# Performance work log

Measured on AMD Instinct MI355X. Metric: run time of the kernel, lower is better.

## Reference

```python
import jax, jax.numpy as jnp
import numpy as np
import math

N_GENES = 5000
N_FREQ = 10
D_EMB = 5
D_SINE = N_FREQ * 2 * 2  # 40


def _sine_consts():
    i = jnp.arange(1, N_FREQ + 1, dtype=jnp.float32)
    freqs = jnp.repeat(1.0 / 1000.0 ** (2.0 * i / N_FREQ), 2)  # [2*n_freq]
    shifts = jnp.tile(jnp.array([0.0, math.pi / 2], dtype=jnp.float32), N_FREQ)  # [2*n_freq]
    return freqs, shifts


def setup_inputs() -> dict:
    key = jax.random.key(0)
    k1, k2, k3 = jax.random.split(key, 3)
    N = 1000000
    coordinates = jax.random.normal(k1, (N, 2), dtype=jnp.float32)
    gene_ix = jax.random.randint(k2, (N,), 0, N_GENES, dtype=jnp.int64) if jax.config.jax_enable_x64 else jax.random.randint(k2, (N,), 0, N_GENES, dtype=jnp.int32)
    stdv = 1.0 / math.sqrt(D_EMB)
    weight1 = jax.random.uniform(k3, (N_GENES, D_SINE, D_EMB), dtype=jnp.float32, minval=-stdv, maxval=stdv)
    bias1 = jnp.zeros((N_GENES, D_EMB), dtype=jnp.float32)
    return {"coordinates": coordinates, "gene_ix": gene_ix, "weight1": weight1, "bias1": bias1}


def reference(coordinates, gene_ix, weight1, bias1):
    freqs, shifts = _sine_consts()
    # [N, 2, 2*n_freq] -> [N, 4*n_freq]
    emb = jnp.sin(coordinates[..., None] * freqs + shifts).reshape(coordinates.shape[0], -1)
    w = weight1[gene_ix]              # [N, D_SINE, D_EMB] gather
    b = bias1[gene_ix]                # [N, D_EMB]
    out = jnp.einsum('ab,abc->ac', emb, w) + b
    return jax.nn.sigmoid(out)
```

## Files before the change

kernel.cpp:

```cpp
#include <hip/hip_runtime.h>
#include <hip/hip_bf16.h>
#include <math.h>


#define N_GENES 5000
#define BLK_BYTES 128
#define W5_BYTES ((size_t)N_GENES * BLK_BYTES)
#define GENES_PER_BLK 51

typedef _Float16 half2_t __attribute__((ext_vector_type(2)));

#if __has_builtin(__builtin_amdgcn_fdot2)
__device__ __forceinline__ float fdot2f(half2_t a, half2_t b, float c) {
    return __builtin_amdgcn_fdot2(a, b, c, false);
}
#else
__device__ __forceinline__ float fdot2f(half2_t a, half2_t b, float c) {
    return fmaf((float)a.x, (float)b.x, fmaf((float)a.y, (float)b.y, c));
}
#endif

__device__ __forceinline__ half2_t pkrtz(float a, float b) {
    auto r = __builtin_amdgcn_cvt_pkrtz(a, b);
    union { decltype(r) s; half2_t d; } v; v.s = r; return v.d;
}
__device__ __forceinline__ half2_t u2h(unsigned int u) {
    union { unsigned int i; half2_t h; } v; v.i = u; return v.h;
}
__device__ __forceinline__ float u2f(unsigned int u) {
    union { unsigned int i; float f; } v; v.i = u; return v.f;
}
__device__ __forceinline__ unsigned int h2u(_Float16 lo, _Float16 hi) {
    union { _Float16 h[2]; unsigned int i; } v; v.h[0] = lo; v.h[1] = hi; return v.i;
}
__device__ __forceinline__ unsigned int f2u(float f) {
    union { float f; unsigned int i; } v; v.f = f; return v.i;
}

__device__ __constant__ float FRc[10] = {
    0.251188643150958f, 0.0630957344480193f, 0.0158489319246111f,
    0.00398107170553497f, 0.001f, 0.000251188643150958f,
    6.30957344480193e-05f, 1.58489319246111e-05f, 3.98107170553497e-06f, 1e-06f
};

__global__ __launch_bounds__(256) void build_w5_lds(
    const float* __restrict__ w,
    const float* __restrict__ bias,
    unsigned char* __restrict__ w5)
{
    __shared__ float lds[GENES_PER_BLK * 200];
    const int g0 = blockIdx.x * GENES_PER_BLK;
    const int ng = (N_GENES - g0 < GENES_PER_BLK) ? (N_GENES - g0) : GENES_PER_BLK;

    const float4* __restrict__ src =
        reinterpret_cast<const float4*>(w + (size_t)g0 * 200);
    const int nf4 = ng * 50;
    for (int k = threadIdx.x; k < nf4; k += 256)
        reinterpret_cast<float4*>(lds)[k] = src[k];
    __syncthreads();

    const int u = threadIdx.x;
    if (u >= ng * 5) return;
    const int gl = u / 5, c = u - 5 * gl;
    const int g = g0 + gl;
    const float* base = lds + gl * 200 + c;

    uint4 S;
    S.x = h2u((_Float16)base[0 * 5],  (_Float16)base[1 * 5]);
    S.y = h2u((_Float16)base[2 * 5],  (_Float16)base[3 * 5]);
    S.z = h2u((_Float16)base[20 * 5], (_Float16)base[21 * 5]);
    S.w = h2u((_Float16)base[22 * 5], (_Float16)base[23 * 5]);

    float Lx = 0.f, Ly = 0.f;
    float bp = bias[(size_t)g * 5 + c];
#pragma unroll
    for (int i = 2; i < 10; ++i) {
        Lx += FRc[i] * base[(2 * i) * 5];
        Ly += FRc[i] * base[(20 + 2 * i) * 5];
        bp += base[(2 * i + 1) * 5] + base[(21 + 2 * i) * 5];
    }

    unsigned char* blk = w5 + (size_t)g * BLK_BYTES;
    *reinterpret_cast<uint4*>(blk + c * 16) = S;
    uint2 L;
    L.x = h2u((_Float16)Lx, (_Float16)Ly);
    L.y = f2u(bp);
    *reinterpret_cast<uint2*>(blk + 80 + c * 8) = L;
}

template <int I>
__device__ __forceinline__ half2_t sc_pack(float x) {
    float t = x * FRc[I];
    float s, co;
    if (I == 0) {
        s  = __sinf(t);
        co = __cosf(t);
    } else {
        float u = t * t;
        s  = t * fmaf(u, fmaf(u, 1.f / 120.f, -1.f / 6.f), 1.f);
        co = fmaf(u, fmaf(u, 1.f / 24.f, -0.5f), 1.f);
    }
    return pkrtz(s, co);
}

__global__ __launch_bounds__(1024) void frag_embed5(
    const float* __restrict__ coords,
    const int*   __restrict__ gene_ix,
    const unsigned char* __restrict__ w5,
    float*       __restrict__ out,
    unsigned int N)
{
    unsigned int tid = blockIdx.x * 1024u + threadIdx.x;
    unsigned int n = tid / 5u;
    unsigned int c = tid - n * 5u;
    if (n >= N) return;

    const float x = coords[2 * (size_t)n];
    const float y = coords[2 * (size_t)n + 1];
    const int g = gene_ix[n];

    const unsigned char* __restrict__ blk = w5 + (size_t)g * BLK_BYTES;
    const uint4 S = *reinterpret_cast<const uint4*>(blk + c * 16);
    const uint2 L = *reinterpret_cast<const uint2*>(blk + 80 + c * 8);

    half2_t sx0 = sc_pack<0>(x), sx1 = sc_pack<1>(x);
    half2_t sy0 = sc_pack<0>(y), sy1 = sc_pack<1>(y);
    half2_t xy  = pkrtz(x, y);

    float acc = u2f(L.y);
    acc = fdot2f(sx0, u2h(S.x), acc);
    acc = fdot2f(sx1, u2h(S.y), acc);
    acc = fdot2f(sy0, u2h(S.z), acc);
    acc = fdot2f(sy1, u2h(S.w), acc);
    acc = fdot2f(xy,  u2h(L.x), acc);

    float r = 1.f / (1.f + __expf(-acc));
    __builtin_nontemporal_store(r, out + (size_t)n * 5 + c);
}

__global__ __launch_bounds__(256) void frag_embed_fallback(
    const float* __restrict__ coords, const int* __restrict__ gene_ix,
    const float* __restrict__ weight, const float* __restrict__ bias,
    float* __restrict__ out, int N)
{
    int n = blockIdx.x * blockDim.x + threadIdx.x;
    if (n >= N) return;
    const float cxo = coords[2 * (size_t)n];
    const float cyo = coords[2 * (size_t)n + 1];
    const int g = gene_ix[n];
    float emb[40];
    float c2[2] = { cxo, cyo };
#pragma unroll
    for (int d = 0; d < 2; ++d)
#pragma unroll
        for (int i = 0; i < 10; ++i) {
            float t = c2[d] * FRc[i];
            emb[d * 20 + 2 * i]     = __sinf(t);
            emb[d * 20 + 2 * i + 1] = __cosf(t);
        }
    const float4* wp = reinterpret_cast<const float4*>(weight + (size_t)g * 200);
    float acc[5];
#pragma unroll
    for (int c = 0; c < 5; ++c) acc[c] = bias[(size_t)g * 5 + c];
#pragma unroll
    for (int j = 0; j < 50; ++j) {
        float4 wv = wp[j];
        const int k = 4 * j;
        acc[(k + 0) % 5] = fmaf(emb[(k + 0) / 5], wv.x, acc[(k + 0) % 5]);
        acc[(k + 1) % 5] = fmaf(emb[(k + 1) / 5], wv.y, acc[(k + 1) % 5]);
        acc[(k + 2) % 5] = fmaf(emb[(k + 2) / 5], wv.z, acc[(k + 2) % 5]);
        acc[(k + 3) % 5] = fmaf(emb[(k + 3) / 5], wv.w, acc[(k + 3) % 5]);
    }
    size_t ob = (size_t)n * 5;
#pragma unroll
    for (int c = 0; c < 5; ++c)
        out[ob + c] = 1.f / (1.f + __expf(-acc[c]));
}

extern "C" void kernel_launch(void* const* d_in, const int* in_sizes, int n_in,
                              void* d_out, int out_size, void* d_ws, size_t ws_size,
                              hipStream_t stream) {
    const float* coords = (const float*)d_in[0];
    const int*   gene   = (const int*)d_in[1];
    const float* w      = (const float*)d_in[2];
    const float* b      = (const float*)d_in[3];
    float*       out    = (float*)d_out;
    const int N = in_sizes[1];

    if (ws_size >= W5_BYTES) {
        unsigned char* w5 = (unsigned char*)d_ws;
        int rblocks = (N_GENES + GENES_PER_BLK - 1) / GENES_PER_BLK;
        build_w5_lds<<<rblocks, 256, 0, stream>>>(w, b, w5);
        long long threads = (long long)N * 5;
        int grid = (int)((threads + 1023) / 1024);
        frag_embed5<<<grid, 1024, 0, stream>>>(coords, gene, w5, out, (unsigned)N);
    } else {
        frag_embed_fallback<<<(N + 255) / 256, 256, 0, stream>>>(coords, gene, w, b, out, N);
    }
}
```

Before: 21.56 us.

## Share per-row sine/cos computation across channel threads via LDS

The main kernel now launches 5x64 thread blocks. Four of the five channel threads per row each compute one sin/cos pair with the hardware intrinsics and write it to shared memory. The other threads read these values after a barrier instead of each computing the sin/cos plus a polynomial approximation itself. Weights and bias are stored negated so the sigmoid becomes rcp(1+exp(acc)) without a negation. The cost is a __syncthreads, LDS traffic, 5-wide thread rows that pack poorly into 64-lane wavefronts, and a precision change: the second frequency now uses __sinf/__cosf instead of the Taylor polynomial.

```diff
diff --git a/kernel.cpp b/kernel.cpp
--- a/kernel.cpp
+++ b/kernel.cpp
@@ -29,6 +29,9 @@
 }
 __device__ __forceinline__ float u2f(unsigned int u) {
     union { unsigned int i; float f; } v; v.i = u; return v.f;
+}
+__device__ __forceinline__ unsigned int h2uu(half2_t h) {
+    union { half2_t h; unsigned int i; } v; v.h = h; return v.i;
 }
 __device__ __forceinline__ unsigned int h2u(_Float16 lo, _Float16 hi) {
     union { _Float16 h[2]; unsigned int i; } v; v.h[0] = lo; v.h[1] = hi; return v.i;
@@ -66,10 +69,10 @@
     const float* base = lds + gl * 200 + c;
 
     uint4 S;
-    S.x = h2u((_Float16)base[0 * 5],  (_Float16)base[1 * 5]);
-    S.y = h2u((_Float16)base[2 * 5],  (_Float16)base[3 * 5]);
-    S.z = h2u((_Float16)base[20 * 5], (_Float16)base[21 * 5]);
-    S.w = h2u((_Float16)base[22 * 5], (_Float16)base[23 * 5]);
+    S.x = h2u((_Float16)(-base[0 * 5]),  (_Float16)(-base[1 * 5]));
+    S.y = h2u((_Float16)(-base[2 * 5]),  (_Float16)(-base[3 * 5]));
+    S.z = h2u((_Float16)(-base[20 * 5]), (_Float16)(-base[21 * 5]));
+    S.w = h2u((_Float16)(-base[22 * 5]), (_Float16)(-base[23 * 5]));
 
     float Lx = 0.f, Ly = 0.f;
     float bp = bias[(size_t)g * 5 + c];
@@ -83,59 +86,57 @@
     unsigned char* blk = w5 + (size_t)g * BLK_BYTES;
     *reinterpret_cast<uint4*>(blk + c * 16) = S;
     uint2 L;
-    L.x = h2u((_Float16)Lx, (_Float16)Ly);
-    L.y = f2u(bp);
+    L.x = h2u((_Float16)(-Lx), (_Float16)(-Ly));
+    L.y = f2u(-bp);
     *reinterpret_cast<uint2*>(blk + 80 + c * 8) = L;
 }
 
-template <int I>
-__device__ __forceinline__ half2_t sc_pack(float x) {
-    float t = x * FRc[I];
-    float s, co;
-    if (I == 0) {
-        s  = __sinf(t);
-        co = __cosf(t);
-    } else {
-        float u = t * t;
-        s  = t * fmaf(u, fmaf(u, 1.f / 120.f, -1.f / 6.f), 1.f);
-        co = fmaf(u, fmaf(u, 1.f / 24.f, -0.5f), 1.f);
-    }
-    return pkrtz(s, co);
-}
-
-__global__ __launch_bounds__(1024) void frag_embed5(
-    const float* __restrict__ coords,
+__global__ __launch_bounds__(320) void frag_embed_sh(
+    const float2* __restrict__ coords,
     const int*   __restrict__ gene_ix,
     const unsigned char* __restrict__ w5,
     float*       __restrict__ out,
     unsigned int N)
 {
-    unsigned int tid = blockIdx.x * 1024u + threadIdx.x;
-    unsigned int n = tid / 5u;
-    unsigned int c = tid - n * 5u;
-    if (n >= N) return;
-
-    const float x = coords[2 * (size_t)n];
-    const float y = coords[2 * (size_t)n + 1];
+    __shared__ unsigned int sinpk[64][4];
+
+    const unsigned int c = threadIdx.x;
+    const unsigned int y = threadIdx.y;
+    unsigned int n = blockIdx.x * 64u + y;
+    const bool valid = (n < N);
+    if (!valid) n = N - 1;
+
+    const float2 xy2 = coords[n];
     const int g = gene_ix[n];
 
     const unsigned char* __restrict__ blk = w5 + (size_t)g * BLK_BYTES;
     const uint4 S = *reinterpret_cast<const uint4*>(blk + c * 16);
     const uint2 L = *reinterpret_cast<const uint2*>(blk + 80 + c * 8);
 
-    half2_t sx0 = sc_pack<0>(x), sx1 = sc_pack<1>(x);
-    half2_t sy0 = sc_pack<0>(y), sy1 = sc_pack<1>(y);
-    half2_t xy  = pkrtz(x, y);
+    {
+        const unsigned int task = c & 3u;
+        const float in = (task & 2u) ? xy2.y : xy2.x;
+        const float fr = (task & 1u) ? FRc[1] : FRc[0];
+        const float t = in * fr;
+        const float s = __sinf(t);
+        const float co = __cosf(t);
+        if (c < 4) sinpk[y][c] = h2uu(pkrtz(s, co));
+    }
+    __syncthreads();
+
+    const uint4 P = *reinterpret_cast<const uint4*>(&sinpk[y][0]);
+    const half2_t xyh = pkrtz(xy2.x, xy2.y);
 
     float acc = u2f(L.y);
-    acc = fdot2f(sx0, u2h(S.x), acc);
-    acc = fdot2f(sx1, u2h(S.y), acc);
-    acc = fdot2f(sy0, u2h(S.z), acc);
-    acc = fdot2f(sy1, u2h(S.w), acc);
-    acc = fdot2f(xy,  u2h(L.x), acc);
-
-    float r = 1.f / (1.f + __expf(-acc));
-    __builtin_nontemporal_store(r, out + (size_t)n * 5 + c);
+    acc = fdot2f(u2h(P.x), u2h(S.x), acc);
+    acc = fdot2f(u2h(P.y), u2h(S.y), acc);
+    acc = fdot2f(u2h(P.z), u2h(S.z), acc);
+    acc = fdot2f(u2h(P.w), u2h(S.w), acc);
+    acc = fdot2f(xyh,      u2h(L.x), acc);
+
+    const float r = __frcp_rn(1.f + __expf(acc));
+    if (valid)
+        __builtin_nontemporal_store(r, out + (size_t)n * 5 + c);
 }
 
 __global__ __launch_bounds__(256) void frag_embed_fallback(
@@ -191,9 +192,10 @@
         unsigned char* w5 = (unsigned char*)d_ws;
         int rblocks = (N_GENES + GENES_PER_BLK - 1) / GENES_PER_BLK;
         build_w5_lds<<<rblocks, 256, 0, stream>>>(w, b, w5);
-        long long threads = (long long)N * 5;
-        int grid = (int)((threads + 1023) / 1024);
-        frag_embed5<<<grid, 1024, 0, stream>>>(coords, gene, w5, out, (unsigned)N);
+        int grid = (N + 63) / 64;
+        dim3 blk(5, 64);
+        frag_embed_sh<<<grid, blk, 0, stream>>>((const float2*)coords, gene, w5,
+                                                out, (unsigned)N);
     } else {
         frag_embed_fallback<<<(N + 255) / 256, 256, 0, stream>>>(coords, gene, w, b, out, N);
     }
```

New measurement: 21.28 us. No clear change (-1.3%).
